# Kernel optimization log

Measured on AMD Instinct MI355X. Metric: run time of the kernel, lower is better.

## Reference

```python
import jax, jax.numpy as jnp
import numpy as np
from jax import lax

B, D, BOND, OUT = 16384, 784, 5, 10

def setup_inputs() -> dict:
    key = jax.random.key(0)
    k = jax.random.split(key, 6)
    x = jax.random.uniform(k[0], (B, D), dtype=jnp.float32)
    core_first = jax.random.normal(k[1], (1, 2, BOND), dtype=jnp.float32) * 0.1
    cores_mid = jax.random.normal(k[2], (D - 2, BOND, 2, BOND), dtype=jnp.float32) * 0.1
    core_last = jax.random.normal(k[3], (BOND, 2, 1), dtype=jnp.float32) * 0.1
    # xavier_uniform for fc.weight with fan_in=1, fan_out=OUT
    bound = float(np.sqrt(6.0 / (1 + OUT)))
    fc_w = jax.random.uniform(k[4], (OUT, 1), dtype=jnp.float32, minval=-bound, maxval=bound)
    fc_b = jnp.zeros((OUT,), dtype=jnp.float32)
    return {"x": x, "core_first": core_first, "cores_mid": cores_mid,
            "core_last": core_last, "fc_w": fc_w, "fc_b": fc_b}

def reference(x, core_first, cores_mid, core_last, fc_w, fc_b):
    # x: [B, D] -> feature map [B, D, 2] = stack(1-x, x)
    xs = jnp.stack([1.0 - x, x], axis=-1)            # [B, D, 2]
    # first core: (1, 2, bond) -> initial carry [B, bond]
    carry0 = jnp.einsum('bi,ir->br', xs[:, 0], core_first[0])  # [B, bond]
    # sequential tensor-train contraction over middle sites via scan
    xs_mid = jnp.moveaxis(xs[:, 1:-1], 1, 0)          # [D-2, B, 2]
    def step(carry, inp):
        xi, core = inp                                # xi: [B,2], core: [bond,2,bond]
        carry = jnp.einsum('bl,bi,lir->br', carry, xi, core)
        return carry, None
    carry, _ = lax.scan(step, carry0, (xs_mid, cores_mid))
    # last core: (bond, 2, 1) -> scalar per batch element
    vlast = jnp.einsum('bi,li->bl', xs[:, -1], core_last[:, :, 0])  # [B, bond]
    res = jnp.sum(carry * vlast, axis=-1, keepdims=True)            # [B, 1]
    out = res @ fc_w.T + fc_b                          # [B, OUT]
    return out
```

## Files before the change

kernel.cpp:

```cpp
#include <hip/hip_runtime.h>


typedef float v4f __attribute__((ext_vector_type(4)));
typedef float v2f __attribute__((ext_vector_type(2)));

constexpr int Bn     = 16384;
constexpr int Dn     = 784;
constexpr int NOUT   = 10;
constexpr int NPAIR  = 390;
constexpr int PFV    = 41;
constexpr int PMAT   = 22;
constexpr int BWD_P0 = 349;
constexpr int PAIR_F = 112;

__device__ __forceinline__ v4f splat4(float x) { v4f v = {x, x, x, x}; return v; }
__device__ __forceinline__ v4f fma4(v4f a, v4f b, v4f c) {
    return __builtin_elementwise_fma(a, b, c);
}

struct Frag { v4f r[5]; float c4[5]; };
struct CMat { v4f row[5]; v4f c4v; float c44; };

__device__ __forceinline__ CMat build_C(const float* s, float xa, float xb) {
    CMat C;
    const float xab = xa * xb;
    const v4f va = splat4(xa), vb = splat4(xb), vab = splat4(xab);
    const v4f* s4 = (const v4f*)s;
#pragma unroll
    for (int l = 0; l < 5; ++l) {
        v4f m = s4[l];
        m = fma4(va,  s4[7 + l],  m);
        m = fma4(vb,  s4[14 + l], m);
        m = fma4(vab, s4[21 + l], m);
        C.row[l] = m;
    }
    {
        v4f m = s4[5];
        m = fma4(va,  s4[12], m);
        m = fma4(vb,  s4[19], m);
        m = fma4(vab, s4[26], m);
        C.c4v = m;
    }
    C.c44 = fmaf(xab, s[108], fmaf(xb, s[80], fmaf(xa, s[52], s[24])));
    return C;
}

__device__ __forceinline__ void matmul(const Frag& M, const CMat& C, Frag& T) {
#pragma unroll
    for (int i = 0; i < 5; ++i) {
        v4f acc  = splat4(M.r[i][0]) * C.row[0];
        float a4 = M.r[i][0] * C.c4v[0];
#pragma unroll
        for (int l = 1; l < 4; ++l) {
            acc = fma4(splat4(M.r[i][l]), C.row[l], acc);
            a4  = fmaf(M.r[i][l], C.c4v[l], a4);
        }
        acc = fma4(splat4(M.c4[i]), C.row[4], acc);
        a4  = fmaf(M.c4[i], C.c44, a4);
        T.r[i] = acc; T.c4[i] = a4;
    }
}

__device__ __forceinline__ void vecstep(v4f& cv, float& c4, const CMat& C) {
    v4f acc  = splat4(cv[0]) * C.row[0];
    float a4 = cv[0] * C.c4v[0];
#pragma unroll
    for (int l = 1; l < 4; ++l) {
        acc = fma4(splat4(cv[l]), C.row[l], acc);
        a4  = fmaf(cv[l], C.c4v[l], a4);
    }
    acc = fma4(splat4(c4), C.row[4], acc);
    a4  = fmaf(c4, C.c44, a4);
    cv = acc; c4 = a4;
}

__device__ __forceinline__ void sload(const v4f* src, v4f& a, v4f& b, int lane) {
    a = src[lane];
    if (lane < 48) b = src[64 + lane];
}
__device__ __forceinline__ void swrite(v4f* dst, v4f a, v4f b, int lane) {
    dst[lane] = a;
    if (lane < 48) dst[64 + lane] = b;
}

__global__ void prepack_pairs(const float* __restrict__ cm, float* __restrict__ pk)
{
    int idx = blockIdx.x * 256 + threadIdx.x;
    if (idx >= NPAIR * 100) return;
    int p = idx / 100, rest = idx - p * 100;
    int q = rest / 25, e = rest - q * 25;
    int l = e / 5, r = e - l * 5;
    int m1 = 2 * p + 1, m2 = 2 * p + 2;
    const float* L = cm + (size_t)(m1 * 5 + l) * 10;
    float acc = 0.f;
#pragma unroll
    for (int k = 0; k < 5; ++k) {
        float Lk = (q & 1) ? (L[5 + k] - L[k]) : L[k];
        const float* R = cm + (size_t)(m2 * 5 + k) * 10;
        float Rk = (q & 2) ? (R[5 + r] - R[r]) : R[r];
        acc = fmaf(Lk, Rk, acc);
    }
    int wl = l, wr = r;
    if (p >= BWD_P0) { wl = r; wr = l; }
    int off = (wr < 4) ? (wl * 4 + wr) : (20 + wl);
    pk[(size_t)p * PAIR_F + q * 28 + off] = acc;
}

__global__ __launch_bounds__(1024, 4)
void mps_pair_kernel(const float* __restrict__ x,
                     const float* __restrict__ core_first,
                     const float* __restrict__ cores_mid,
                     const float* __restrict__ core_last,
                     const float* __restrict__ fc_w,
                     const float* __restrict__ fc_b,
                     const float* __restrict__ pk,
                     float* __restrict__ out)
{
    __shared__ v4f   pkbuf[16][2][112];
    __shared__ float matbuf[7][25][64];
    __shared__ float bv[5][64];

    const int lane = threadIdx.x & 63;
    const int wave = threadIdx.x >> 6;
    const int row  = blockIdx.x * 64 + lane;
    const float* __restrict__ xr = x + (size_t)row * Dn;
    const v2f* __restrict__ xr2 = (const v2f*)xr;
    const v4f* __restrict__ pk4 = (const v4f*)pk;

    v4f* buf0 = &pkbuf[wave][0][0];
    v4f* buf1 = &pkbuf[wave][1][0];

    if (wave >= 1 && wave <= 14) {
        const int w  = wave;
        const int p0 = PFV + PMAT * (w - 1);
        v4f sa, sb;
        sload(pk4 + (size_t)p0 * 28, sa, sb, lane);
        swrite(buf0, sa, sb, lane);
        sload(pk4 + (size_t)(p0 + 4) * 28, sa, sb, lane);
        v2f xc0 = xr2[p0 + 1], xc1 = xr2[p0 + 2], xc2 = xr2[p0 + 3], xc3 = xr2[p0 + 4];

        Frag M, T;
        M.r[0] = {1,0,0,0}; M.r[1] = {0,1,0,0}; M.r[2] = {0,0,1,0};
        M.r[3] = {0,0,0,1}; M.r[4] = {0,0,0,0};
        M.c4[0] = 0; M.c4[1] = 0; M.c4[2] = 0; M.c4[3] = 0; M.c4[4] = 1;

#pragma unroll 1
        for (int c = 0; c < 6; ++c) {
            v4f* wb = (c & 1) ? buf0 : buf1;
            const float* rb = (const float*)((c & 1) ? buf1 : buf0);
            swrite(wb, sa, sb, lane);
            int ns = p0 + 4 * (c + 2);
            if (ns > NPAIR - 4) ns = NPAIR - 4;
            sload(pk4 + (size_t)ns * 28, sa, sb, lane);
            const int pn = p0 + 4 * (c + 1);
            v2f xn0 = xr2[pn + 1], xn1 = xr2[pn + 2], xn2 = xr2[pn + 3], xn3 = xr2[pn + 4];
            {
                CMat C = build_C(rb + 0 * PAIR_F, xc0[0], xc0[1]);
                matmul(M, C, T);
                C = build_C(rb + 1 * PAIR_F, xc1[0], xc1[1]);
                matmul(T, C, M);
            }
            if (c < 5) {
                CMat C = build_C(rb + 2 * PAIR_F, xc2[0], xc2[1]);
                matmul(M, C, T);
                C = build_C(rb + 3 * PAIR_F, xc3[0], xc3[1]);
                matmul(T, C, M);
            }
            xc0 = xn0; xc1 = xn1; xc2 = xn2; xc3 = xn3;
        }

        if (w <= 7) {
#pragma unroll
            for (int i = 0; i < 5; ++i) {
#pragma unroll
                for (int r = 0; r < 4; ++r) matbuf[w - 1][i * 5 + r][lane] = M.r[i][r];
                matbuf[w - 1][i * 5 + 4][lane] = M.c4[i];
            }
        }
        __syncthreads();
        __syncthreads();
        if (w >= 8) {
#pragma unroll
            for (int i = 0; i < 5; ++i) {
#pragma unroll
                for (int r = 0; r < 4; ++r) matbuf[w - 8][i * 5 + r][lane] = M.r[i][r];
                matbuf[w - 8][i * 5 + 4][lane] = M.c4[i];
            }
        }
        __syncthreads();
    } else if (wave == 0) {
        v2f x01 = xr2[0];
        float cl[5], cn[5];
#pragma unroll
        for (int r = 0; r < 5; ++r)
            cl[r] = fmaf(x01[0], core_first[5 + r] - core_first[r], core_first[r]);
        const float* cm0 = cores_mid;
#pragma unroll
        for (int r = 0; r < 5; ++r) {
            float a = 0.f;
#pragma unroll
            for (int l = 0; l < 5; ++l) {
                float m = fmaf(x01[1], cm0[l * 10 + 5 + r] - cm0[l * 10 + r], cm0[l * 10 + r]);
                a = fmaf(cl[l], m, a);
            }
            cn[r] = a;
        }
        v4f cv = {cn[0], cn[1], cn[2], cn[3]};
        float c4 = cn[4];

        v4f sa, sb;
        sload(pk4 + 0, sa, sb, lane);
        swrite(buf0, sa, sb, lane);
        sload(pk4 + (size_t)4 * 28, sa, sb, lane);
        v2f xc0 = xr2[1], xc1 = xr2[2], xc2 = xr2[3], xc3 = xr2[4];

#pragma unroll 1
        for (int c = 0; c < 11; ++c) {
            v4f* wb = (c & 1) ? buf0 : buf1;
            const float* rb = (const float*)((c & 1) ? buf1 : buf0);
            swrite(wb, sa, sb, lane);
            int ns = 4 * (c + 2);
            if (ns > NPAIR - 4) ns = NPAIR - 4;
            sload(pk4 + (size_t)ns * 28, sa, sb, lane);
            const int pn = 4 * (c + 1);
            v2f xn0 = xr2[pn + 1], xn1 = xr2[pn + 2], xn2 = xr2[pn + 3], xn3 = xr2[pn + 4];
            {
                CMat C = build_C(rb + 0 * PAIR_F, xc0[0], xc0[1]);
                vecstep(cv, c4, C);
            }
            if (c < 10) {
                CMat C = build_C(rb + 1 * PAIR_F, xc1[0], xc1[1]);
                vecstep(cv, c4, C);
                C = build_C(rb + 2 * PAIR_F, xc2[0], xc2[1]);
                vecstep(cv, c4, C);
                C = build_C(rb + 3 * PAIR_F, xc3[0], xc3[1]);
                vecstep(cv, c4, C);
            }
            xc0 = xn0; xc1 = xn1; xc2 = xn2; xc3 = xn3;
        }
        cl[0] = cv[0]; cl[1] = cv[1]; cl[2] = cv[2]; cl[3] = cv[3]; cl[4] = c4;

        __syncthreads();
#pragma unroll 1
        for (int w2 = 0; w2 < 7; ++w2) {
            float v0[5];
#pragma unroll
            for (int r = 0; r < 5; ++r) v0[r] = cl[0] * matbuf[w2][r][lane];
#pragma unroll
            for (int l = 1; l < 5; ++l)
#pragma unroll
                for (int r = 0; r < 5; ++r)
                    v0[r] = fmaf(cl[l], matbuf[w2][l * 5 + r][lane], v0[r]);
#pragma unroll
            for (int r = 0; r < 5; ++r) cl[r] = v0[r];
        }
        __syncthreads();
        __syncthreads();
#pragma unroll 1
        for (int w2 = 0; w2 < 7; ++w2) {
            float v0[5];
#pragma unroll
            for (int r = 0; r < 5; ++r) v0[r] = cl[0] * matbuf[w2][r][lane];
#pragma unroll
            for (int l = 1; l < 5; ++l)
#pragma unroll
                for (int r = 0; r < 5; ++r)
                    v0[r] = fmaf(cl[l], matbuf[w2][l * 5 + r][lane], v0[r]);
#pragma unroll
            for (int r = 0; r < 5; ++r) cl[r] = v0[r];
        }
        float res = 0.f;
#pragma unroll
        for (int l = 0; l < 5; ++l) res = fmaf(cl[l], bv[l][lane], res);
        float* orow = out + (size_t)row * NOUT;
#pragma unroll
        for (int o = 0; o < NOUT; ++o) orow[o] = fmaf(res, fc_w[o], fc_b[o]);
    } else {
        v2f xz = xr2[391];
        float vl[5], vn[5];
#pragma unroll
        for (int l = 0; l < 5; ++l)
            vl[l] = fmaf(xz[1], core_last[2 * l + 1] - core_last[2 * l], core_last[2 * l]);
        const float* cmL = cores_mid + (size_t)781 * 50;
#pragma unroll
        for (int l = 0; l < 5; ++l) {
            float a = 0.f;
#pragma unroll
            for (int r = 0; r < 5; ++r) {
                float m = fmaf(xz[0], cmL[l * 10 + 5 + r] - cmL[l * 10 + r], cmL[l * 10 + r]);
                a = fmaf(m, vl[r], a);
            }
            vn[l] = a;
        }
        v4f cv = {vn[0], vn[1], vn[2], vn[3]};
        float c4 = vn[4];

        v4f sa, sb;
        sload(pk4 + (size_t)386 * 28, sa, sb, lane);
        swrite(buf0, sa, sb, lane);
        sload(pk4 + (size_t)382 * 28, sa, sb, lane);
        v2f xc0 = xr2[390], xc1 = xr2[389], xc2 = xr2[388], xc3 = xr2[387];

#pragma unroll 1
        for (int c = 0; c < 11; ++c) {
            v4f* wb = (c & 1) ? buf0 : buf1;
            const float* rb = (const float*)((c & 1) ? buf1 : buf0);
            swrite(wb, sa, sb, lane);
            int ns = 386 - 4 * (c + 2);
            sload(pk4 + (size_t)ns * 28, sa, sb, lane);
            const int bn = 386 - 4 * (c + 1);
            v2f xn0 = xr2[bn + 4], xn1 = xr2[bn + 3], xn2 = xr2[bn + 2], xn3 = xr2[bn + 1];
            {
                CMat C = build_C(rb + 3 * PAIR_F, xc0[0], xc0[1]);
                vecstep(cv, c4, C);
            }
            if (c < 10) {
                CMat C = build_C(rb + 2 * PAIR_F, xc1[0], xc1[1]);
                vecstep(cv, c4, C);
                C = build_C(rb + 1 * PAIR_F, xc2[0], xc2[1]);
                vecstep(cv, c4, C);
                C = build_C(rb + 0 * PAIR_F, xc3[0], xc3[1]);
                vecstep(cv, c4, C);
            }
            xc0 = xn0; xc1 = xn1; xc2 = xn2; xc3 = xn3;
        }

        __syncthreads();
        __syncthreads();
        bv[0][lane] = cv[0]; bv[1][lane] = cv[1]; bv[2][lane] = cv[2];
        bv[3][lane] = cv[3]; bv[4][lane] = c4;
        __syncthreads();
    }
}

extern "C" void kernel_launch(void* const* d_in, const int* in_sizes, int n_in,
                              void* d_out, int out_size, void* d_ws, size_t ws_size,
                              hipStream_t stream) {
    const float* x          = (const float*)d_in[0];
    const float* core_first = (const float*)d_in[1];
    const float* cores_mid  = (const float*)d_in[2];
    const float* core_last  = (const float*)d_in[3];
    const float* fc_w       = (const float*)d_in[4];
    const float* fc_b       = (const float*)d_in[5];
    float* out              = (float*)d_out;
    float* pk               = (float*)d_ws;

    hipLaunchKernelGGL(prepack_pairs, dim3((NPAIR * 100 + 255) / 256), dim3(256),
                       0, stream, cores_mid, pk);
    hipLaunchKernelGGL(mps_pair_kernel, dim3(Bn / 64), dim3(1024), 0, stream,
                       x, core_first, cores_mid, core_last, fc_w, fc_b, pk, out);
}
```

Measured before the change: 125.8 us.

## Split chain across two blocks, two rows per thread, finish in separate kernel

Restructures the tensor-train contraction so each block handles only half the chain (left or right) for 128 rows. Each thread carries two batch rows, which amortises the shared-memory core loads and the build of the contracted matrix over both rows. The pair-core packing is compacted from 112 to 100 floats. The two half results are written into the output buffer as scratch and combined by a new small kernel that applies the final linear layer. This trades an extra kernel launch and a global round trip, plus higher register pressure from the doubled state, for fewer waves per block and less redundant staging of the core matrices.

```diff
diff --git a/kernel.cpp b/kernel.cpp
--- a/kernel.cpp
+++ b/kernel.cpp
@@ -8,10 +8,12 @@
 constexpr int Dn     = 784;
 constexpr int NOUT   = 10;
 constexpr int NPAIR  = 390;
-constexpr int PFV    = 41;
+constexpr int PVEC   = 41;
 constexpr int PMAT   = 22;
+constexpr int RHP0   = 195;
 constexpr int BWD_P0 = 349;
-constexpr int PAIR_F = 112;
+constexpr int PAIR_F = 100;
+constexpr int PAIR_V = 25;
 
 __device__ __forceinline__ v4f splat4(float x) { v4f v = {x, x, x, x}; return v; }
 __device__ __forceinline__ v4f fma4(v4f a, v4f b, v4f c) {
@@ -21,28 +23,29 @@
 struct Frag { v4f r[5]; float c4[5]; };
 struct CMat { v4f row[5]; v4f c4v; float c44; };
 
-__device__ __forceinline__ CMat build_C(const float* s, float xa, float xb) {
-    CMat C;
-    const float xab = xa * xb;
-    const v4f va = splat4(xa), vb = splat4(xb), vab = splat4(xab);
+__device__ __forceinline__ void build_C2(const float* s, v2f xA, v2f xB,
+                                         CMat& CA, CMat& CB) {
+    const float aA = xA[0], bA = xA[1], pA = aA * bA;
+    const float aB = xB[0], bB = xB[1], pB = aB * bB;
+    const v4f vaA = splat4(aA), vbA = splat4(bA), vpA = splat4(pA);
+    const v4f vaB = splat4(aB), vbB = splat4(bB), vpB = splat4(pB);
     const v4f* s4 = (const v4f*)s;
 #pragma unroll
     for (int l = 0; l < 5; ++l) {
-        v4f m = s4[l];
-        m = fma4(va,  s4[7 + l],  m);
-        m = fma4(vb,  s4[14 + l], m);
-        m = fma4(vab, s4[21 + l], m);
-        C.row[l] = m;
+        v4f q0 = s4[l], q1 = s4[5 + l], q2 = s4[10 + l], q3 = s4[15 + l];
+        CA.row[l] = fma4(vpA, q3, fma4(vbA, q2, fma4(vaA, q1, q0)));
+        CB.row[l] = fma4(vpB, q3, fma4(vbB, q2, fma4(vaB, q1, q0)));
     }
     {
-        v4f m = s4[5];
-        m = fma4(va,  s4[12], m);
-        m = fma4(vb,  s4[19], m);
-        m = fma4(vab, s4[26], m);
-        C.c4v = m;
-    }
-    C.c44 = fmaf(xab, s[108], fmaf(xb, s[80], fmaf(xa, s[52], s[24])));
-    return C;
+        v4f q0 = s4[20], q1 = s4[21], q2 = s4[22], q3 = s4[23];
+        CA.c4v = fma4(vpA, q3, fma4(vbA, q2, fma4(vaA, q1, q0)));
+        CB.c4v = fma4(vpB, q3, fma4(vbB, q2, fma4(vaB, q1, q0)));
+    }
+    {
+        v4f q = s4[24];
+        CA.c44 = fmaf(pA, q[3], fmaf(bA, q[2], fmaf(aA, q[1], q[0])));
+        CB.c44 = fmaf(pB, q[3], fmaf(bB, q[2], fmaf(aB, q[1], q[0])));
+    }
 }
 
 __device__ __forceinline__ void matmul(const Frag& M, const CMat& C, Frag& T) {
@@ -76,11 +79,11 @@
 
 __device__ __forceinline__ void sload(const v4f* src, v4f& a, v4f& b, int lane) {
     a = src[lane];
-    if (lane < 48) b = src[64 + lane];
+    if (lane < 36) b = src[64 + lane];
 }
 __device__ __forceinline__ void swrite(v4f* dst, v4f a, v4f b, int lane) {
     dst[lane] = a;
-    if (lane < 48) dst[64 + lane] = b;
+    if (lane < 36) dst[64 + lane] = b;
 }
 
 __global__ void prepack_pairs(const float* __restrict__ cm, float* __restrict__ pk)
@@ -102,47 +105,55 @@
     }
     int wl = l, wr = r;
     if (p >= BWD_P0) { wl = r; wr = l; }
-    int off = (wr < 4) ? (wl * 4 + wr) : (20 + wl);
-    pk[(size_t)p * PAIR_F + q * 28 + off] = acc;
-}
-
-__global__ __launch_bounds__(1024, 4)
-void mps_pair_kernel(const float* __restrict__ x,
+    int off;
+    if (wr < 4)      off = q * 20 + wl * 4 + wr;
+    else if (wl < 4) off = 80 + q * 4 + wl;
+    else             off = 96 + q;
+    pk[(size_t)p * PAIR_F + off] = acc;
+}
+
+__global__ __launch_bounds__(512, 2)
+void mps_half_kernel(const float* __restrict__ x,
                      const float* __restrict__ core_first,
                      const float* __restrict__ cores_mid,
                      const float* __restrict__ core_last,
-                     const float* __restrict__ fc_w,
-                     const float* __restrict__ fc_b,
                      const float* __restrict__ pk,
                      float* __restrict__ out)
 {
-    __shared__ v4f   pkbuf[16][2][112];
-    __shared__ float matbuf[7][25][64];
-    __shared__ float bv[5][64];
+    __shared__ v4f   pkbuf[8][2][100];
+    __shared__ float matbuf[7][25][128];
 
     const int lane = threadIdx.x & 63;
     const int wave = threadIdx.x >> 6;
-    const int row  = blockIdx.x * 64 + lane;
-    const float* __restrict__ xr = x + (size_t)row * Dn;
-    const v2f* __restrict__ xr2 = (const v2f*)xr;
+    const int g    = blockIdx.x >> 1;
+    const int h    = blockIdx.x & 1;
+    const int rowA = g * 128 + lane;
+    const int rowB = rowA + 64;
+    const v2f* __restrict__ xA2 = (const v2f*)(x + (size_t)rowA * Dn);
+    const v2f* __restrict__ xB2 = (const v2f*)(x + (size_t)rowB * Dn);
     const v4f* __restrict__ pk4 = (const v4f*)pk;
 
     v4f* buf0 = &pkbuf[wave][0][0];
     v4f* buf1 = &pkbuf[wave][1][0];
 
-    if (wave >= 1 && wave <= 14) {
-        const int w  = wave;
-        const int p0 = PFV + PMAT * (w - 1);
+    const bool isvec = (h == 0) ? (wave == 0) : (wave == 7);
+
+    if (!isvec) {
+        const int slot = (h == 0) ? (wave - 1) : wave;
+        const int p0   = (h == 0) ? (PVEC + PMAT * (wave - 1))
+                                  : (RHP0 + PMAT * wave);
         v4f sa, sb;
-        sload(pk4 + (size_t)p0 * 28, sa, sb, lane);
+        sload(pk4 + (size_t)p0 * PAIR_V, sa, sb, lane);
         swrite(buf0, sa, sb, lane);
-        sload(pk4 + (size_t)(p0 + 4) * 28, sa, sb, lane);
-        v2f xc0 = xr2[p0 + 1], xc1 = xr2[p0 + 2], xc2 = xr2[p0 + 3], xc3 = xr2[p0 + 4];
-
-        Frag M, T;
-        M.r[0] = {1,0,0,0}; M.r[1] = {0,1,0,0}; M.r[2] = {0,0,1,0};
-        M.r[3] = {0,0,0,1}; M.r[4] = {0,0,0,0};
-        M.c4[0] = 0; M.c4[1] = 0; M.c4[2] = 0; M.c4[3] = 0; M.c4[4] = 1;
+        sload(pk4 + (size_t)(p0 + 4) * PAIR_V, sa, sb, lane);
+        v2f cA0 = xA2[p0 + 1], cA1 = xA2[p0 + 2], cA2 = xA2[p0 + 3], cA3 = xA2[p0 + 4];
+        v2f cB0 = xB2[p0 + 1], cB1 = xB2[p0 + 2], cB2 = xB2[p0 + 3], cB3 = xB2[p0 + 4];
+
+        Frag MA, TA, MB, TB;
+        MA.r[0] = {1,0,0,0}; MA.r[1] = {0,1,0,0}; MA.r[2] = {0,0,1,0};
+        MA.r[3] = {0,0,0,1}; MA.r[4] = {0,0,0,0};
+        MA.c4[0] = 0; MA.c4[1] = 0; MA.c4[2] = 0; MA.c4[3] = 0; MA.c4[4] = 1;
+        MB = MA;
 
 #pragma unroll 1
         for (int c = 0; c < 6; ++c) {
@@ -151,68 +162,67 @@
             swrite(wb, sa, sb, lane);
             int ns = p0 + 4 * (c + 2);
             if (ns > NPAIR - 4) ns = NPAIR - 4;
-            sload(pk4 + (size_t)ns * 28, sa, sb, lane);
+            sload(pk4 + (size_t)ns * PAIR_V, sa, sb, lane);
             const int pn = p0 + 4 * (c + 1);
-            v2f xn0 = xr2[pn + 1], xn1 = xr2[pn + 2], xn2 = xr2[pn + 3], xn3 = xr2[pn + 4];
-            {
-                CMat C = build_C(rb + 0 * PAIR_F, xc0[0], xc0[1]);
-                matmul(M, C, T);
-                C = build_C(rb + 1 * PAIR_F, xc1[0], xc1[1]);
-                matmul(T, C, M);
-            }
+            v2f nA0 = xA2[pn + 1], nA1 = xA2[pn + 2], nA2 = xA2[pn + 3], nA3 = xA2[pn + 4];
+            v2f nB0 = xB2[pn + 1], nB1 = xB2[pn + 2], nB2 = xB2[pn + 3], nB3 = xB2[pn + 4];
+            CMat CA, CB;
+            build_C2(rb + 0 * PAIR_F, cA0, cB0, CA, CB);
+            matmul(MA, CA, TA); matmul(MB, CB, TB);
+            build_C2(rb + 1 * PAIR_F, cA1, cB1, CA, CB);
+            matmul(TA, CA, MA); matmul(TB, CB, MB);
             if (c < 5) {
-                CMat C = build_C(rb + 2 * PAIR_F, xc2[0], xc2[1]);
-                matmul(M, C, T);
-                C = build_C(rb + 3 * PAIR_F, xc3[0], xc3[1]);
-                matmul(T, C, M);
-            }
-            xc0 = xn0; xc1 = xn1; xc2 = xn2; xc3 = xn3;
-        }
-
-        if (w <= 7) {
-#pragma unroll
-            for (int i = 0; i < 5; ++i) {
-#pragma unroll
-                for (int r = 0; r < 4; ++r) matbuf[w - 1][i * 5 + r][lane] = M.r[i][r];
-                matbuf[w - 1][i * 5 + 4][lane] = M.c4[i];
-            }
+                build_C2(rb + 2 * PAIR_F, cA2, cB2, CA, CB);
+                matmul(MA, CA, TA); matmul(MB, CB, TB);
+                build_C2(rb + 3 * PAIR_F, cA3, cB3, CA, CB);
+                matmul(TA, CA, MA); matmul(TB, CB, MB);
+            }
+            cA0 = nA0; cA1 = nA1; cA2 = nA2; cA3 = nA3;
+            cB0 = nB0; cB1 = nB1; cB2 = nB2; cB3 = nB3;
+        }
+
+#pragma unroll
+        for (int i = 0; i < 5; ++i) {
+#pragma unroll
+            for (int r = 0; r < 4; ++r) {
+                matbuf[slot][i * 5 + r][lane]      = MA.r[i][r];
+                matbuf[slot][i * 5 + r][lane + 64] = MB.r[i][r];
+            }
+            matbuf[slot][i * 5 + 4][lane]      = MA.c4[i];
+            matbuf[slot][i * 5 + 4][lane + 64] = MB.c4[i];
         }
         __syncthreads();
-        __syncthreads();
-        if (w >= 8) {
-#pragma unroll
-            for (int i = 0; i < 5; ++i) {
-#pragma unroll
-                for (int r = 0; r < 4; ++r) matbuf[w - 8][i * 5 + r][lane] = M.r[i][r];
-                matbuf[w - 8][i * 5 + 4][lane] = M.c4[i];
-            }
-        }
-        __syncthreads();
-    } else if (wave == 0) {
-        v2f x01 = xr2[0];
-        float cl[5], cn[5];
-#pragma unroll
-        for (int r = 0; r < 5; ++r)
-            cl[r] = fmaf(x01[0], core_first[5 + r] - core_first[r], core_first[r]);
+    } else if (h == 0) {
+        v2f xA01 = xA2[0], xB01 = xB2[0];
+        float clA[5], clB[5], cnA[5], cnB[5];
+#pragma unroll
+        for (int r = 0; r < 5; ++r) {
+            float d = core_first[5 + r] - core_first[r];
+            clA[r] = fmaf(xA01[0], d, core_first[r]);
+            clB[r] = fmaf(xB01[0], d, core_first[r]);
+        }
         const float* cm0 = cores_mid;
 #pragma unroll
         for (int r = 0; r < 5; ++r) {
-            float a = 0.f;
+            float aA = 0.f, aB = 0.f;
 #pragma unroll
             for (int l = 0; l < 5; ++l) {
-                float m = fmaf(x01[1], cm0[l * 10 + 5 + r] - cm0[l * 10 + r], cm0[l * 10 + r]);
-                a = fmaf(cl[l], m, a);
-            }
-            cn[r] = a;
-        }
-        v4f cv = {cn[0], cn[1], cn[2], cn[3]};
-        float c4 = cn[4];
+                float base = cm0[l * 10 + r], d = cm0[l * 10 + 5 + r] - base;
+                aA = fmaf(clA[l], fmaf(xA01[1], d, base), aA);
+                aB = fmaf(clB[l], fmaf(xB01[1], d, base), aB);
+            }
+            cnA[r] = aA; cnB[r] = aB;
+        }
+        v4f cvA = {cnA[0], cnA[1], cnA[2], cnA[3]};
+        v4f cvB = {cnB[0], cnB[1], cnB[2], cnB[3]};
+        float c4A = cnA[4], c4B = cnB[4];
 
         v4f sa, sb;
         sload(pk4 + 0, sa, sb, lane);
         swrite(buf0, sa, sb, lane);
-        sload(pk4 + (size_t)4 * 28, sa, sb, lane);
-        v2f xc0 = xr2[1], xc1 = xr2[2], xc2 = xr2[3], xc3 = xr2[4];
+        sload(pk4 + (size_t)4 * PAIR_V, sa, sb, lane);
+        v2f cA0 = xA2[1], cA1 = xA2[2], cA2 = xA2[3], cA3 = xA2[4];
+        v2f cB0 = xB2[1], cB1 = xB2[2], cB2 = xB2[3], cB3 = xB2[4];
 
 #pragma unroll 1
         for (int c = 0; c < 11; ++c) {
@@ -221,85 +231,81 @@
             swrite(wb, sa, sb, lane);
             int ns = 4 * (c + 2);
             if (ns > NPAIR - 4) ns = NPAIR - 4;
-            sload(pk4 + (size_t)ns * 28, sa, sb, lane);
+            sload(pk4 + (size_t)ns * PAIR_V, sa, sb, lane);
             const int pn = 4 * (c + 1);
-            v2f xn0 = xr2[pn + 1], xn1 = xr2[pn + 2], xn2 = xr2[pn + 3], xn3 = xr2[pn + 4];
-            {
-                CMat C = build_C(rb + 0 * PAIR_F, xc0[0], xc0[1]);
-                vecstep(cv, c4, C);
-            }
+            v2f nA0 = xA2[pn + 1], nA1 = xA2[pn + 2], nA2 = xA2[pn + 3], nA3 = xA2[pn + 4];
+            v2f nB0 = xB2[pn + 1], nB1 = xB2[pn + 2], nB2 = xB2[pn + 3], nB3 = xB2[pn + 4];
+            CMat CA, CB;
+            build_C2(rb + 0 * PAIR_F, cA0, cB0, CA, CB);
+            vecstep(cvA, c4A, CA); vecstep(cvB, c4B, CB);
             if (c < 10) {
-                CMat C = build_C(rb + 1 * PAIR_F, xc1[0], xc1[1]);
-                vecstep(cv, c4, C);
-                C = build_C(rb + 2 * PAIR_F, xc2[0], xc2[1]);
-                vecstep(cv, c4, C);
-                C = build_C(rb + 3 * PAIR_F, xc3[0], xc3[1]);
-                vecstep(cv, c4, C);
-            }
-            xc0 = xn0; xc1 = xn1; xc2 = xn2; xc3 = xn3;
-        }
-        cl[0] = cv[0]; cl[1] = cv[1]; cl[2] = cv[2]; cl[3] = cv[3]; cl[4] = c4;
+                build_C2(rb + 1 * PAIR_F, cA1, cB1, CA, CB);
+                vecstep(cvA, c4A, CA); vecstep(cvB, c4B, CB);
+                build_C2(rb + 2 * PAIR_F, cA2, cB2, CA, CB);
+                vecstep(cvA, c4A, CA); vecstep(cvB, c4B, CB);
+                build_C2(rb + 3 * PAIR_F, cA3, cB3, CA, CB);
+                vecstep(cvA, c4A, CA); vecstep(cvB, c4B, CB);
+            }
+            cA0 = nA0; cA1 = nA1; cA2 = nA2; cA3 = nA3;
+            cB0 = nB0; cB1 = nB1; cB2 = nB2; cB3 = nB3;
+        }
+        clA[0] = cvA[0]; clA[1] = cvA[1]; clA[2] = cvA[2]; clA[3] = cvA[3]; clA[4] = c4A;
+        clB[0] = cvB[0]; clB[1] = cvB[1]; clB[2] = cvB[2]; clB[3] = cvB[3]; clB[4] = c4B;
 
         __syncthreads();
 #pragma unroll 1
         for (int w2 = 0; w2 < 7; ++w2) {
-            float v0[5];
-#pragma unroll
-            for (int r = 0; r < 5; ++r) v0[r] = cl[0] * matbuf[w2][r][lane];
+            float vA[5], vB[5];
+#pragma unroll
+            for (int r = 0; r < 5; ++r) {
+                vA[r] = clA[0] * matbuf[w2][r][lane];
+                vB[r] = clB[0] * matbuf[w2][r][lane + 64];
+            }
 #pragma unroll
             for (int l = 1; l < 5; ++l)
 #pragma unroll
-                for (int r = 0; r < 5; ++r)
-                    v0[r] = fmaf(cl[l], matbuf[w2][l * 5 + r][lane], v0[r]);
-#pragma unroll
-            for (int r = 0; r < 5; ++r) cl[r] = v0[r];
-        }
-        __syncthreads();
-        __syncthreads();
-#pragma unroll 1
-        for (int w2 = 0; w2 < 7; ++w2) {
-            float v0[5];
-#pragma unroll
-            for (int r = 0; r < 5; ++r) v0[r] = cl[0] * matbuf[w2][r][lane];
-#pragma unroll
-            for (int l = 1; l < 5; ++l)
-#pragma unroll
-                for (int r = 0; r < 5; ++r)
-                    v0[r] = fmaf(cl[l], matbuf[w2][l * 5 + r][lane], v0[r]);
-#pragma unroll
-            for (int r = 0; r < 5; ++r) cl[r] = v0[r];
-        }
-        float res = 0.f;
-#pragma unroll
-        for (int l = 0; l < 5; ++l) res = fmaf(cl[l], bv[l][lane], res);
-        float* orow = out + (size_t)row * NOUT;
-#pragma unroll
-        for (int o = 0; o < NOUT; ++o) orow[o] = fmaf(res, fc_w[o], fc_b[o]);
+                for (int r = 0; r < 5; ++r) {
+                    vA[r] = fmaf(clA[l], matbuf[w2][l * 5 + r][lane],      vA[r]);
+                    vB[r] = fmaf(clB[l], matbuf[w2][l * 5 + r][lane + 64], vB[r]);
+                }
+#pragma unroll
+            for (int r = 0; r < 5; ++r) { clA[r] = vA[r]; clB[r] = vB[r]; }
+        }
+        float* oA = out + (size_t)rowA * NOUT;
+        float* oB = out + (size_t)rowB * NOUT;
+#pragma unroll
+        for (int i = 0; i < 5; ++i) { oA[i] = clA[i]; oB[i] = clB[i]; }
     } else {
-        v2f xz = xr2[391];
-        float vl[5], vn[5];
-#pragma unroll
-        for (int l = 0; l < 5; ++l)
-            vl[l] = fmaf(xz[1], core_last[2 * l + 1] - core_last[2 * l], core_last[2 * l]);
+        v2f xAz = xA2[391], xBz = xB2[391];
+        float vlA[5], vlB[5], vnA[5], vnB[5];
+#pragma unroll
+        for (int l = 0; l < 5; ++l) {
+            float base = core_last[2 * l], d = core_last[2 * l + 1] - base;
+            vlA[l] = fmaf(xAz[1], d, base);
+            vlB[l] = fmaf(xBz[1], d, base);
+        }
         const float* cmL = cores_mid + (size_t)781 * 50;
 #pragma unroll
         for (int l = 0; l < 5; ++l) {
-            float a = 0.f;
+            float aA = 0.f, aB = 0.f;
 #pragma unroll
             for (int r = 0; r < 5; ++r) {
-                float m = fmaf(xz[0], cmL[l * 10 + 5 + r] - cmL[l * 10 + r], cmL[l * 10 + r]);
-                a = fmaf(m, vl[r], a);
-            }
-            vn[l] = a;
-        }
-        v4f cv = {vn[0], vn[1], vn[2], vn[3]};
-        float c4 = vn[4];
+                float base = cmL[l * 10 + r], d = cmL[l * 10 + 5 + r] - base;
+                aA = fmaf(fmaf(xAz[0], d, base), vlA[r], aA);
+                aB = fmaf(fmaf(xBz[0], d, base), vlB[r], aB);
+            }
+            vnA[l] = aA; vnB[l] = aB;
+        }
+        v4f cvA = {vnA[0], vnA[1], vnA[2], vnA[3]};
+        v4f cvB = {vnB[0], vnB[1], vnB[2], vnB[3]};
+        float c4A = vnA[4], c4B = vnB[4];
 
         v4f sa, sb;
-        sload(pk4 + (size_t)386 * 28, sa, sb, lane);
+        sload(pk4 + (size_t)386 * PAIR_V, sa, sb, lane);
         swrite(buf0, sa, sb, lane);
-        sload(pk4 + (size_t)382 * 28, sa, sb, lane);
-        v2f xc0 = xr2[390], xc1 = xr2[389], xc2 = xr2[388], xc3 = xr2[387];
+        sload(pk4 + (size_t)382 * PAIR_V, sa, sb, lane);
+        v2f cA0 = xA2[390], cA1 = xA2[389], cA2 = xA2[388], cA3 = xA2[387];
+        v2f cB0 = xB2[390], cB1 = xB2[389], cB2 = xB2[388], cB3 = xB2[387];
 
 #pragma unroll 1
         for (int c = 0; c < 11; ++c) {
@@ -307,30 +313,70 @@
             const float* rb = (const float*)((c & 1) ? buf1 : buf0);
             swrite(wb, sa, sb, lane);
             int ns = 386 - 4 * (c + 2);
-            sload(pk4 + (size_t)ns * 28, sa, sb, lane);
+            sload(pk4 + (size_t)ns * PAIR_V, sa, sb, lane);
             const int bn = 386 - 4 * (c + 1);
-            v2f xn0 = xr2[bn + 4], xn1 = xr2[bn + 3], xn2 = xr2[bn + 2], xn3 = xr2[bn + 1];
-            {
-                CMat C = build_C(rb + 3 * PAIR_F, xc0[0], xc0[1]);
-                vecstep(cv, c4, C);
-            }
+            v2f nA0 = xA2[bn + 4], nA1 = xA2[bn + 3], nA2 = xA2[bn + 2], nA3 = xA2[bn + 1];
+            v2f nB0 = xB2[bn + 4], nB1 = xB2[bn + 3], nB2 = xB2[bn + 2], nB3 = xB2[bn + 1];
+            CMat CA, CB;
+            build_C2(rb + 3 * PAIR_F, cA0, cB0, CA, CB);
+            vecstep(cvA, c4A, CA); vecstep(cvB, c4B, CB);
             if (c < 10) {
-                CMat C = build_C(rb + 2 * PAIR_F, xc1[0], xc1[1]);
-                vecstep(cv, c4, C);
-                C = build_C(rb + 1 * PAIR_F, xc2[0], xc2[1]);
-                vecstep(cv, c4, C);
-                C = build_C(rb + 0 * PAIR_F, xc3[0], xc3[1]);
-                vecstep(cv, c4, C);
-            }
-            xc0 = xn0; xc1 = xn1; xc2 = xn2; xc3 = xn3;
-        }
+                build_C2(rb + 2 * PAIR_F, cA1, cB1, CA, CB);
+                vecstep(cvA, c4A, CA); vecstep(cvB, c4B, CB);
+                build_C2(rb + 1 * PAIR_F, cA2, cB2, CA, CB);
+                vecstep(cvA, c4A, CA); vecstep(cvB, c4B, CB);
+                build_C2(rb + 0 * PAIR_F, cA3, cB3, CA, CB);
+                vecstep(cvA, c4A, CA); vecstep(cvB, c4B, CB);
+            }
+            cA0 = nA0; cA1 = nA1; cA2 = nA2; cA3 = nA3;
+            cB0 = nB0; cB1 = nB1; cB2 = nB2; cB3 = nB3;
+        }
+        float uA[5] = {cvA[0], cvA[1], cvA[2], cvA[3], c4A};
+        float uB[5] = {cvB[0], cvB[1], cvB[2], cvB[3], c4B};
 
         __syncthreads();
-        __syncthreads();
-        bv[0][lane] = cv[0]; bv[1][lane] = cv[1]; bv[2][lane] = cv[2];
-        bv[3][lane] = cv[3]; bv[4][lane] = c4;
-        __syncthreads();
-    }
+#pragma unroll 1
+        for (int w2 = 6; w2 >= 0; --w2) {
+            float vA[5], vB[5];
+#pragma unroll
+            for (int i = 0; i < 5; ++i) {
+                float aA = matbuf[w2][i * 5][lane]      * uA[0];
+                float aB = matbuf[w2][i * 5][lane + 64] * uB[0];
+#pragma unroll
+                for (int l = 1; l < 5; ++l) {
+                    aA = fmaf(matbuf[w2][i * 5 + l][lane],      uA[l], aA);
+                    aB = fmaf(matbuf[w2][i * 5 + l][lane + 64], uB[l], aB);
+                }
+                vA[i] = aA; vB[i] = aB;
+            }
+#pragma unroll
+            for (int i = 0; i < 5; ++i) { uA[i] = vA[i]; uB[i] = vB[i]; }
+        }
+        float* oA = out + (size_t)rowA * NOUT;
+        float* oB = out + (size_t)rowB * NOUT;
+#pragma unroll
+        for (int i = 0; i < 5; ++i) { oA[5 + i] = uA[i]; oB[5 + i] = uB[i]; }
+    }
+}
+
+__global__ __launch_bounds__(256)
+void finish_out(const float* __restrict__ fc_w, const float* __restrict__ fc_b,
+                float* __restrict__ out)
+{
+    int row = blockIdx.x * 256 + threadIdx.x;
+    float* o = out + (size_t)row * NOUT;
+    v2f e0 = *(const v2f*)(o + 0);
+    v2f e1 = *(const v2f*)(o + 2);
+    v2f e2 = *(const v2f*)(o + 4);
+    v2f e3 = *(const v2f*)(o + 6);
+    v2f e4 = *(const v2f*)(o + 8);
+    float res = e0[0] * e2[1];
+    res = fmaf(e0[1], e3[0], res);
+    res = fmaf(e1[0], e3[1], res);
+    res = fmaf(e1[1], e4[0], res);
+    res = fmaf(e2[0], e4[1], res);
+#pragma unroll
+    for (int j = 0; j < NOUT; ++j) o[j] = fmaf(res, fc_w[j], fc_b[j]);
 }
 
 extern "C" void kernel_launch(void* const* d_in, const int* in_sizes, int n_in,
@@ -347,6 +393,8 @@
 
     hipLaunchKernelGGL(prepack_pairs, dim3((NPAIR * 100 + 255) / 256), dim3(256),
                        0, stream, cores_mid, pk);
-    hipLaunchKernelGGL(mps_pair_kernel, dim3(Bn / 64), dim3(1024), 0, stream,
-                       x, core_first, cores_mid, core_last, fc_w, fc_b, pk, out);
-}
+    hipLaunchKernelGGL(mps_half_kernel, dim3(256), dim3(512), 0, stream,
+                       x, core_first, cores_mid, core_last, pk, out);
+    hipLaunchKernelGGL(finish_out, dim3(Bn / 256), dim3(256), 0, stream,
+                       fc_w, fc_b, out);
+}
```

Measured after the change: 148.6 us. 18.1% more time.

## Read packed pair cores directly from global memory with uniform wave index

Applied to the files above, without the earlier changes.

Drops the per-wave LDS double-buffered staging of packed pair-core data. Each step now reads coefficients straight from global memory through a wave-uniform pointer (readfirstlane on the wave index), so they can be fetched as scalar or broadcast loads. The packed layout shrinks from 112 to 100 floats with the q-interleaved last-column terms, and the C-matrix build is fused into the matmul one row at a time to cut register pressure. In exchange it relies on scalar-cache hits and loses the explicit prefetch pipelining.

```diff
diff --git a/kernel.cpp b/kernel.cpp
--- a/kernel.cpp
+++ b/kernel.cpp
@@ -11,7 +11,7 @@
 constexpr int PFV    = 41;
 constexpr int PMAT   = 22;
 constexpr int BWD_P0 = 349;
-constexpr int PAIR_F = 112;
+constexpr int PAIR_F = 100;
 
 __device__ __forceinline__ v4f splat4(float x) { v4f v = {x, x, x, x}; return v; }
 __device__ __forceinline__ v4f fma4(v4f a, v4f b, v4f c) {
@@ -19,68 +19,47 @@
 }
 
 struct Frag { v4f r[5]; float c4[5]; };
-struct CMat { v4f row[5]; v4f c4v; float c44; };
-
-__device__ __forceinline__ CMat build_C(const float* s, float xa, float xb) {
-    CMat C;
-    const float xab = xa * xb;
-    const v4f va = splat4(xa), vb = splat4(xb), vab = splat4(xab);
+
+__device__ __forceinline__ void matstepLM(const Frag& M, Frag& T,
+                                          const float* __restrict__ s, v2f xc) {
+    const float xa = xc[0], xb = xc[1], xab = xa * xb;
+    const v4f va = splat4(xa), vb = splat4(xb), vp = splat4(xab);
     const v4f* s4 = (const v4f*)s;
 #pragma unroll
     for (int l = 0; l < 5; ++l) {
-        v4f m = s4[l];
-        m = fma4(va,  s4[7 + l],  m);
-        m = fma4(vb,  s4[14 + l], m);
-        m = fma4(vab, s4[21 + l], m);
-        C.row[l] = m;
-    }
-    {
-        v4f m = s4[5];
-        m = fma4(va,  s4[12], m);
-        m = fma4(vb,  s4[19], m);
-        m = fma4(vab, s4[26], m);
-        C.c4v = m;
-    }
-    C.c44 = fmaf(xab, s[108], fmaf(xb, s[80], fmaf(xa, s[52], s[24])));
-    return C;
-}
-
-__device__ __forceinline__ void matmul(const Frag& M, const CMat& C, Frag& T) {
-#pragma unroll
-    for (int i = 0; i < 5; ++i) {
-        v4f acc  = splat4(M.r[i][0]) * C.row[0];
-        float a4 = M.r[i][0] * C.c4v[0];
-#pragma unroll
-        for (int l = 1; l < 4; ++l) {
-            acc = fma4(splat4(M.r[i][l]), C.row[l], acc);
-            a4  = fmaf(M.r[i][l], C.c4v[l], a4);
-        }
-        acc = fma4(splat4(M.c4[i]), C.row[4], acc);
-        a4  = fmaf(M.c4[i], C.c44, a4);
-        T.r[i] = acc; T.c4[i] = a4;
-    }
-}
-
-__device__ __forceinline__ void vecstep(v4f& cv, float& c4, const CMat& C) {
-    v4f acc  = splat4(cv[0]) * C.row[0];
-    float a4 = cv[0] * C.c4v[0];
-#pragma unroll
-    for (int l = 1; l < 4; ++l) {
-        acc = fma4(splat4(cv[l]), C.row[l], acc);
-        a4  = fmaf(cv[l], C.c4v[l], a4);
-    }
-    acc = fma4(splat4(c4), C.row[4], acc);
-    a4  = fmaf(c4, C.c44, a4);
+        v4f crow = fma4(vp, s4[15 + l], fma4(vb, s4[10 + l], fma4(va, s4[5 + l], s4[l])));
+        v4f cq = (l < 4) ? s4[20 + l] : s4[24];
+        float c4l = fmaf(xab, cq[3], fmaf(xb, cq[2], fmaf(xa, cq[1], cq[0])));
+#pragma unroll
+        for (int i = 0; i < 5; ++i) {
+            float mil = (l < 4) ? M.r[i][l] : M.c4[i];
+            if (l == 0) {
+                T.r[i]  = splat4(mil) * crow;
+                T.c4[i] = mil * c4l;
+            } else {
+                T.r[i]  = fma4(splat4(mil), crow, T.r[i]);
+                T.c4[i] = fmaf(mil, c4l, T.c4[i]);
+            }
+        }
+    }
+}
+
+__device__ __forceinline__ void vecstepLM(v4f& cv, float& c4,
+                                          const float* __restrict__ s, v2f xc) {
+    const float xa = xc[0], xb = xc[1], xab = xa * xb;
+    const v4f va = splat4(xa), vb = splat4(xb), vp = splat4(xab);
+    const v4f* s4 = (const v4f*)s;
+    v4f acc; float a4;
+#pragma unroll
+    for (int l = 0; l < 5; ++l) {
+        v4f crow = fma4(vp, s4[15 + l], fma4(vb, s4[10 + l], fma4(va, s4[5 + l], s4[l])));
+        v4f cq = (l < 4) ? s4[20 + l] : s4[24];
+        float c4l = fmaf(xab, cq[3], fmaf(xb, cq[2], fmaf(xa, cq[1], cq[0])));
+        float cl = (l < 4) ? cv[l] : c4;
+        if (l == 0) { acc = splat4(cl) * crow; a4 = cl * c4l; }
+        else        { acc = fma4(splat4(cl), crow, acc); a4 = fmaf(cl, c4l, a4); }
+    }
     cv = acc; c4 = a4;
-}
-
-__device__ __forceinline__ void sload(const v4f* src, v4f& a, v4f& b, int lane) {
-    a = src[lane];
-    if (lane < 48) b = src[64 + lane];
-}
-__device__ __forceinline__ void swrite(v4f* dst, v4f a, v4f b, int lane) {
-    dst[lane] = a;
-    if (lane < 48) dst[64 + lane] = b;
 }
 
 __global__ void prepack_pairs(const float* __restrict__ cm, float* __restrict__ pk)
@@ -102,8 +81,11 @@
     }
     int wl = l, wr = r;
     if (p >= BWD_P0) { wl = r; wr = l; }
-    int off = (wr < 4) ? (wl * 4 + wr) : (20 + wl);
-    pk[(size_t)p * PAIR_F + q * 28 + off] = acc;
+    int off;
+    if (wr < 4)      off = q * 20 + wl * 4 + wr;
+    else if (wl < 4) off = 80 + wl * 4 + q;
+    else             off = 96 + q;
+    pk[(size_t)p * PAIR_F + off] = acc;
 }
 
 __global__ __launch_bounds__(1024, 4)
@@ -116,79 +98,54 @@
                      const float* __restrict__ pk,
                      float* __restrict__ out)
 {
-    __shared__ v4f   pkbuf[16][2][112];
     __shared__ float matbuf[7][25][64];
     __shared__ float bv[5][64];
 
     const int lane = threadIdx.x & 63;
     const int wave = threadIdx.x >> 6;
+    const int wu   = __builtin_amdgcn_readfirstlane(wave);
     const int row  = blockIdx.x * 64 + lane;
     const float* __restrict__ xr = x + (size_t)row * Dn;
     const v2f* __restrict__ xr2 = (const v2f*)xr;
-    const v4f* __restrict__ pk4 = (const v4f*)pk;
-
-    v4f* buf0 = &pkbuf[wave][0][0];
-    v4f* buf1 = &pkbuf[wave][1][0];
-
-    if (wave >= 1 && wave <= 14) {
-        const int w  = wave;
-        const int p0 = PFV + PMAT * (w - 1);
-        v4f sa, sb;
-        sload(pk4 + (size_t)p0 * 28, sa, sb, lane);
-        swrite(buf0, sa, sb, lane);
-        sload(pk4 + (size_t)(p0 + 4) * 28, sa, sb, lane);
-        v2f xc0 = xr2[p0 + 1], xc1 = xr2[p0 + 2], xc2 = xr2[p0 + 3], xc3 = xr2[p0 + 4];
+
+    if (wu >= 1 && wu <= 14) {
+        const int p0 = PFV + PMAT * (wu - 1);
 
         Frag M, T;
         M.r[0] = {1,0,0,0}; M.r[1] = {0,1,0,0}; M.r[2] = {0,0,1,0};
         M.r[3] = {0,0,0,1}; M.r[4] = {0,0,0,0};
         M.c4[0] = 0; M.c4[1] = 0; M.c4[2] = 0; M.c4[3] = 0; M.c4[4] = 1;
 
-#pragma unroll 1
-        for (int c = 0; c < 6; ++c) {
-            v4f* wb = (c & 1) ? buf0 : buf1;
-            const float* rb = (const float*)((c & 1) ? buf1 : buf0);
-            swrite(wb, sa, sb, lane);
-            int ns = p0 + 4 * (c + 2);
-            if (ns > NPAIR - 4) ns = NPAIR - 4;
-            sload(pk4 + (size_t)ns * 28, sa, sb, lane);
-            const int pn = p0 + 4 * (c + 1);
-            v2f xn0 = xr2[pn + 1], xn1 = xr2[pn + 2], xn2 = xr2[pn + 3], xn3 = xr2[pn + 4];
-            {
-                CMat C = build_C(rb + 0 * PAIR_F, xc0[0], xc0[1]);
-                matmul(M, C, T);
-                C = build_C(rb + 1 * PAIR_F, xc1[0], xc1[1]);
-                matmul(T, C, M);
-            }
-            if (c < 5) {
-                CMat C = build_C(rb + 2 * PAIR_F, xc2[0], xc2[1]);
-                matmul(M, C, T);
-                C = build_C(rb + 3 * PAIR_F, xc3[0], xc3[1]);
-                matmul(T, C, M);
-            }
-            xc0 = xn0; xc1 = xn1; xc2 = xn2; xc3 = xn3;
-        }
-
-        if (w <= 7) {
+        v2f x0 = xr2[p0 + 1], x1 = xr2[p0 + 2];
+#pragma unroll 1
+        for (int j = 0; j < PMAT; j += 2) {
+            const float* s0 = pk + (size_t)(p0 + j) * PAIR_F;
+            v2f nx0 = xr2[p0 + j + 3], nx1 = xr2[p0 + j + 4];
+            matstepLM(M, T, s0, x0);
+            matstepLM(T, M, s0 + PAIR_F, x1);
+            x0 = nx0; x1 = nx1;
+        }
+
+        if (wu <= 7) {
 #pragma unroll
             for (int i = 0; i < 5; ++i) {
 #pragma unroll
-                for (int r = 0; r < 4; ++r) matbuf[w - 1][i * 5 + r][lane] = M.r[i][r];
-                matbuf[w - 1][i * 5 + 4][lane] = M.c4[i];
-            }
-        }
-        __syncthreads();
-        __syncthreads();
-        if (w >= 8) {
+                for (int r = 0; r < 4; ++r) matbuf[wu - 1][i * 5 + r][lane] = M.r[i][r];
+                matbuf[wu - 1][i * 5 + 4][lane] = M.c4[i];
+            }
+        }
+        __syncthreads();
+        __syncthreads();
+        if (wu >= 8) {
 #pragma unroll
             for (int i = 0; i < 5; ++i) {
 #pragma unroll
-                for (int r = 0; r < 4; ++r) matbuf[w - 8][i * 5 + r][lane] = M.r[i][r];
-                matbuf[w - 8][i * 5 + 4][lane] = M.c4[i];
-            }
-        }
-        __syncthreads();
-    } else if (wave == 0) {
+                for (int r = 0; r < 4; ++r) matbuf[wu - 8][i * 5 + r][lane] = M.r[i][r];
+                matbuf[wu - 8][i * 5 + 4][lane] = M.c4[i];
+            }
+        }
+        __syncthreads();
+    } else if (wu == 0) {
         v2f x01 = xr2[0];
         float cl[5], cn[5];
 #pragma unroll
@@ -208,35 +165,12 @@
         v4f cv = {cn[0], cn[1], cn[2], cn[3]};
         float c4 = cn[4];
 
-        v4f sa, sb;
-        sload(pk4 + 0, sa, sb, lane);
-        swrite(buf0, sa, sb, lane);
-        sload(pk4 + (size_t)4 * 28, sa, sb, lane);
-        v2f xc0 = xr2[1], xc1 = xr2[2], xc2 = xr2[3], xc3 = xr2[4];
-
-#pragma unroll 1
-        for (int c = 0; c < 11; ++c) {
-            v4f* wb = (c & 1) ? buf0 : buf1;
-            const float* rb = (const float*)((c & 1) ? buf1 : buf0);
-            swrite(wb, sa, sb, lane);
-            int ns = 4 * (c + 2);
-            if (ns > NPAIR - 4) ns = NPAIR - 4;
-            sload(pk4 + (size_t)ns * 28, sa, sb, lane);
-            const int pn = 4 * (c + 1);
-            v2f xn0 = xr2[pn + 1], xn1 = xr2[pn + 2], xn2 = xr2[pn + 3], xn3 = xr2[pn + 4];
-            {
-                CMat C = build_C(rb + 0 * PAIR_F, xc0[0], xc0[1]);
-                vecstep(cv, c4, C);
-            }
-            if (c < 10) {
-                CMat C = build_C(rb + 1 * PAIR_F, xc1[0], xc1[1]);
-                vecstep(cv, c4, C);
-                C = build_C(rb + 2 * PAIR_F, xc2[0], xc2[1]);
-                vecstep(cv, c4, C);
-                C = build_C(rb + 3 * PAIR_F, xc3[0], xc3[1]);
-                vecstep(cv, c4, C);
-            }
-            xc0 = xn0; xc1 = xn1; xc2 = xn2; xc3 = xn3;
+        v2f xc = xr2[1];
+#pragma unroll 1
+        for (int p = 0; p < PFV; ++p) {
+            v2f nx = xr2[p + 2];
+            vecstepLM(cv, c4, pk + (size_t)p * PAIR_F, xc);
+            xc = nx;
         }
         cl[0] = cv[0]; cl[1] = cv[1]; cl[2] = cv[2]; cl[3] = cv[3]; cl[4] = c4;
 
@@ -295,34 +229,12 @@
         v4f cv = {vn[0], vn[1], vn[2], vn[3]};
         float c4 = vn[4];
 
-        v4f sa, sb;
-        sload(pk4 + (size_t)386 * 28, sa, sb, lane);
-        swrite(buf0, sa, sb, lane);
-        sload(pk4 + (size_t)382 * 28, sa, sb, lane);
-        v2f xc0 = xr2[390], xc1 = xr2[389], xc2 = xr2[388], xc3 = xr2[387];
-
-#pragma unroll 1
-        for (int c = 0; c < 11; ++c) {
-            v4f* wb = (c & 1) ? buf0 : buf1;
-            const float* rb = (const float*)((c & 1) ? buf1 : buf0);
-            swrite(wb, sa, sb, lane);
-            int ns = 386 - 4 * (c + 2);
-            sload(pk4 + (size_t)ns * 28, sa, sb, lane);
-            const int bn = 386 - 4 * (c + 1);
-            v2f xn0 = xr2[bn + 4], xn1 = xr2[bn + 3], xn2 = xr2[bn + 2], xn3 = xr2[bn + 1];
-            {
-                CMat C = build_C(rb + 3 * PAIR_F, xc0[0], xc0[1]);
-                vecstep(cv, c4, C);
-            }
-            if (c < 10) {
-                CMat C = build_C(rb + 2 * PAIR_F, xc1[0], xc1[1]);
-                vecstep(cv, c4, C);
-                C = build_C(rb + 1 * PAIR_F, xc2[0], xc2[1]);
-                vecstep(cv, c4, C);
-                C = build_C(rb + 0 * PAIR_F, xc3[0], xc3[1]);
-                vecstep(cv, c4, C);
-            }
-            xc0 = xn0; xc1 = xn1; xc2 = xn2; xc3 = xn3;
+        v2f xc = xr2[390];
+#pragma unroll 1
+        for (int p = 389; p >= BWD_P0; --p) {
+            v2f nx = xr2[p];
+            vecstepLM(cv, c4, pk + (size_t)p * PAIR_F, xc);
+            xc = nx;
         }
 
         __syncthreads();
```

Result: no change. 125.0 us (-0.6%).
